# Kernel optimization log

Hardware: AMD Instinct MI355X
Metric: run time of the kernel (lower is better)

## Reference

```python
import jax, jax.numpy as jnp
import numpy as np
from math import factorial, pi, sqrt

N_ATOMS = 4096
N_PAIRS = 49152
F = 16           # num_tensordense_features
NUM_RADIAL = 16  # basis num=16
NUM_SPECIES = 95
EMB_DIM = 32
CUTOFF = 5.0
LMAX = 4         # SelfAttention max_degree=4
NLM = 25
LMAX_B = 2       # basis max_degree=2 (also max_tensordense_degree)
NLM_B = 9

DEG9 = np.repeat(np.arange(3), [1, 3, 5])        # degree index of each lm, l<=2
DEG25 = np.repeat(np.arange(5), [1, 3, 5, 7, 9]) # degree index of each lm, l<=4


def real_sph(u, lmax):
    # real spherical harmonics (m = -l..l ordering, no Condon-Shortley), u: (...,3) unit vectors
    x, y, z = u[..., 0], u[..., 1], u[..., 2]
    phi = jnp.arctan2(y, x)
    ct = jnp.clip(z, -1.0, 1.0)
    st = jnp.sqrt(jnp.clip(1.0 - ct * ct, 0.0, 1.0))
    P = {(0, 0): jnp.ones_like(ct)}
    for m in range(1, lmax + 1):
        P[(m, m)] = -(2 * m - 1) * st * P[(m - 1, m - 1)]
    for m in range(0, lmax):
        P[(m + 1, m)] = (2 * m + 1) * ct * P[(m, m)]
    for m in range(0, lmax + 1):
        for l in range(m + 2, lmax + 1):
            P[(l, m)] = ((2 * l - 1) * ct * P[(l - 1, m)] - (l + m - 1) * P[(l - 2, m)]) / (l - m)
    outs = []
    for l in range(lmax + 1):
        for m in range(-l, l + 1):
            ma = abs(m)
            Nn = sqrt((2 * l + 1) / (4 * pi) * factorial(l - ma) / factorial(l + ma))
            cs = (-1.0) ** ma  # cancel Condon-Shortley in P
            if m == 0:
                Y = Nn * P[(l, 0)]
            elif m > 0:
                Y = sqrt(2.0) * Nn * cs * jnp.cos(m * phi) * P[(l, m)]
            else:
                Y = sqrt(2.0) * Nn * cs * jnp.sin(ma * phi) * P[(l, ma)]
            outs.append(Y)
    return jnp.stack(outs, axis=-1)


def _gaunt():
    # exact real Gaunt (CG-equivalent) coupling coefficients via Gauss-Legendre x uniform-phi quadrature
    nt, nph = 16, 32
    xs, ws = np.polynomial.legendre.leggauss(nt)
    phis = np.arange(nph) * (2 * np.pi / nph)
    ct = np.repeat(xs, nph); ph = np.tile(phis, nt)
    st = np.sqrt(np.clip(1.0 - ct ** 2, 0.0, 1.0))
    u = np.stack([st * np.cos(ph), st * np.sin(ph), ct], -1)
    w = np.repeat(ws, nph) * (2 * np.pi / nph)
    Y = np.asarray(real_sph(jnp.asarray(u, dtype=jnp.float32), LMAX))
    G = np.einsum('gi,gj,gk,g->ijk', Y, Y[:, :NLM_B], Y, w)
    G[np.abs(G) < 1e-6] = 0.0
    return G

_G = _gaunt()
G_ATT = jnp.asarray(_G, dtype=jnp.float32)                      # (25, 9, 25): feat x basis -> feat
G_TD = jnp.asarray(_G[:NLM_B, :, :NLM_B], dtype=jnp.float32)    # (9, 9, 9): TensorDense coupling


def pdense(x, W, deg):
    return jnp.einsum('plf,lfg->plg', x, W[deg])


def couple(xf, Bf, G):
    # equivariant tensor product  out[p,k,f] = sum_ij G[i,j,k] xf[p,i,f] Bf[p,j,f]
    u = jnp.einsum('pif,ijk->pjkf', xf, G)
    return jnp.einsum('pjf,pjkf->pkf', Bf, u)


def setup_inputs() -> dict:
    key = jax.random.key(0)
    ks = jax.random.split(key, 24)
    s = 1.0 / np.sqrt(F)
    inp = dict(
        atomic_numbers=jax.random.randint(ks[0], (N_ATOMS,), 0, NUM_SPECIES),
        neighbour_indices=jnp.stack([
            jax.random.randint(ks[1], (N_PAIRS,), 0, N_ATOMS),
            jax.random.randint(ks[2], (N_PAIRS,), 0, N_ATOMS)], axis=-1),
        neighbour_displacements=jax.random.normal(ks[3], (N_PAIRS, 3), dtype=jnp.float32) * 1.7,
        W_rad=jax.random.normal(ks[4], (NUM_SPECIES, NUM_RADIAL, F), dtype=jnp.float32) / np.sqrt(NUM_RADIAL),
        emb_table=jax.random.normal(ks[5], (NUM_SPECIES, EMB_DIM), dtype=jnp.float32),
        W_emb=jax.random.normal(ks[6], (EMB_DIM, F), dtype=jnp.float32) / np.sqrt(EMB_DIM),
        b_emb=jnp.zeros((F,), jnp.float32),
        td_W1=jax.random.normal(ks[7], (3, F, F), dtype=jnp.float32) * s,
        td_W2=jax.random.normal(ks[8], (3, F, F), dtype=jnp.float32) * s,
        td_W3=jax.random.normal(ks[9], (3, F, F), dtype=jnp.float32) * s,
        Wb1=jax.random.normal(ks[10], (NUM_RADIAL, F), dtype=jnp.float32) / np.sqrt(NUM_RADIAL),
        Wq1=jax.random.normal(ks[11], (5, F, F), dtype=jnp.float32) * s,
        Wk1=jax.random.normal(ks[12], (5, F, F), dtype=jnp.float32) * s,
        Wv1=jax.random.normal(ks[13], (5, F, F), dtype=jnp.float32) * s,
        Wo1=jax.random.normal(ks[14], (5, F, F), dtype=jnp.float32) * s,
        bo1=jnp.zeros((F,), jnp.float32),
        Wb2=jax.random.normal(ks[15], (NUM_RADIAL, F), dtype=jnp.float32) / np.sqrt(NUM_RADIAL),
        Wq2=jax.random.normal(ks[16], (5, F, F), dtype=jnp.float32) * s,
        Wk2=jax.random.normal(ks[17], (5, F, F), dtype=jnp.float32) * s,
        Wv2=jax.random.normal(ks[18], (5, F, F), dtype=jnp.float32) * s,
        Wo2=jax.random.normal(ks[19], (5, F, F), dtype=jnp.float32) * s,
        bo2=jnp.zeros((F,), jnp.float32),
    )
    return inp


def reference(atomic_numbers, neighbour_indices, neighbour_displacements,
              W_rad, emb_table, W_emb, b_emb, td_W1, td_W2, td_W3,
              Wb1, Wq1, Wk1, Wv1, Wo1, bo1, Wb2, Wq2, Wk2, Wv2, Wo2, bo2):
    dst = neighbour_indices[:, 0]   # idx_i
    src = neighbour_indices[:, 1]   # idx_j
    Zj = atomic_numbers[src]
    r = jnp.linalg.norm(neighbour_displacements, axis=-1)
    u = neighbour_displacements / jnp.maximum(r, 1e-9)[:, None]
    sh = real_sph(u, LMAX)          # (P, 25)
    sh_b = sh[:, :NLM_B]            # (P, 9)
    kk = jnp.arange(1, NUM_RADIAL + 1, dtype=jnp.float32)
    rb = jnp.sinc(kk[None, :] * r[:, None] / CUTOFF) * (r < CUTOFF)[:, None]  # sinc basis w/ cutoff
    # species-aware radial basis -> per-pair equivariant features (P, 9, F)
    y0 = jnp.einsum('pk,pkf->pf', rb, W_rad[Zj])
    y = sh_b[:, :, None] * y0[:, None, :]
    # TensorDense: dense -> CG tensor product -> dense (degrees <= 2)
    a = pdense(y, td_W1, DEG9)
    b = pdense(y, td_W2, DEG9)
    u9 = jnp.einsum('pif,ijk->pjkf', a, G_TD)
    tp = jnp.einsum('pjf,pjkf->pkf', b, u9)
    y = pdense(tp, td_W3, DEG9)
    # aggregate per-pair messages to atoms (segment mean), pad degrees to l<=4
    sums = jnp.zeros((N_ATOMS, NLM_B, F), y.dtype).at[dst].add(y)
    cnt = jnp.zeros((N_ATOMS,), y.dtype).at[dst].add(1.0)
    x = sums / jnp.maximum(cnt, 1.0)[:, None, None]
    x = jnp.pad(x, ((0, 0), (0, NLM - NLM_B), (0, 0)))  # (N, 25, F)
    # two segment self-attention layers over neighbour pairs
    for (Wb, Wq, Wk, Wv, Wo, bo) in ((Wb1, Wq1, Wk1, Wv1, Wo1, bo1), (Wb2, Wq2, Wk2, Wv2, Wo2, bo2)):
        Bf = sh_b[:, :, None] * (rb @ Wb)[:, None, :]   # projected pair basis (P, 9, F)
        q = pdense(x, Wq, DEG25)[dst]
        kf = couple(pdense(x, Wk, DEG25)[src], Bf, G_ATT)
        vf = couple(pdense(x, Wv, DEG25)[src], Bf, G_ATT)
        s = jnp.einsum('plf,plf->p', q, kf) / np.sqrt(NLM * F)
        m = jax.lax.stop_gradient(jnp.full((N_ATOMS,), -1e30, s.dtype).at[dst].max(s))
        e = jnp.exp(s - m[dst])
        den = jnp.zeros((N_ATOMS,), s.dtype).at[dst].add(e)
        alpha = e / (den[dst] + 1e-9)
        agg = jnp.zeros((N_ATOMS, NLM, F), x.dtype).at[dst].add(alpha[:, None, None] * vf)
        x = pdense(agg, Wo, DEG25)
        x = x.at[:, 0, :].add(bo)
    # embedding residual connection on the scalar (l=0) channel
    res = emb_table[atomic_numbers] @ W_emb + b_emb
    x = x.at[:, 0, :].add(res)
    return x
```

## Files before the change

### kernel.cpp

```cpp
#include <hip/hip_runtime.h>
#include <hip/hip_bf16.h>

#define NA 4096
#define NP 49152

typedef _Float16 f16;
typedef _Float16 h2 __attribute__((ext_vector_type(2)));
union U4H { uint4 u; f16 h[8]; h2 p[4]; };

__device__ __forceinline__ float fdot2(h2 a, h2 b, float c){
#if __has_builtin(__builtin_amdgcn_fdot2)
  return __builtin_amdgcn_fdot2(a, b, c, false);
#else
  return c + (float)a.x*(float)b.x + (float)a.y*(float)b.y;
#endif
}

constexpr int WS_AOFS9 = 64;
constexpr int WS_ATTW9 = 128;
constexpr int WS_ATTIJ9= WS_ATTW9 + 512;
constexpr int WS_G     = 12800;
constexpr int WS_NATT  = WS_G + 5632;
constexpr int WS_ATTW  = WS_NATT + 8;
constexpr int WS_ATTIJ = WS_ATTW + 1024;
constexpr int WS_TDOFS = WS_ATTIJ + 1024;
constexpr int WS_TDW   = WS_TDOFS + 16;
constexpr int WS_TDIJ  = WS_TDW + 512;
constexpr int WS_AOFS  = WS_TDIJ + 512;
constexpr int WS_SH    = WS_AOFS + 32;
constexpr int WS_RB    = WS_SH + NP*9;
constexpr int WS_S     = WS_RB + NP*16;
constexpr int WS_CCNT  = WS_S + NP;
constexpr int WS_COFF  = WS_CCNT + NA;
constexpr int WS_CCUR  = WS_COFF + NA + 8;
constexpr int WS_CLST  = WS_CCUR + NA;
constexpr int WS_XQ    = WS_CLST + NP;
constexpr int WS_XK    = WS_XQ + NA*400;
constexpr int WS_XV    = WS_XK + NA*400;
constexpr int WS_PVF   = WS_XV + NA*400;
constexpr int WS_WW    = WS_PVF + NP*128;
constexpr int WS_PVFE  = WS_PVF + NP*256;
constexpr int WS_DS    = WS_PVFE;
constexpr long long WS_END = (long long)WS_DS + 2*NP + 16;

__device__ const float  GLX[16] = {
  -0.98940093499164993f, -0.94457502307323258f, -0.86563120238783174f, -0.75540440835500303f,
  -0.61787624440264375f, -0.45801677765722739f, -0.28160355077925891f, -0.09501250983763744f,
   0.09501250983763744f,  0.28160355077925891f,  0.45801677765722739f,  0.61787624440264375f,
   0.75540440835500303f,  0.86563120238783174f,  0.94457502307323258f,  0.98940093499164993f };
__device__ const double GLW[16] = {
  0.02715245941175409, 0.06225352393864789, 0.09515851168249278, 0.12462897125553387,
  0.14959598881657673, 0.16915651939500254, 0.18260341504492359, 0.18945061045506850,
  0.18945061045506850, 0.18260341504492359, 0.16915651939500254, 0.14959598881657673,
  0.12462897125553387, 0.09515851168249278, 0.06225352393864789, 0.02715245941175409 };

#define PI_D 3.14159265358979323846

__device__ __forceinline__ float scrub(float v){
  if(!(v == v)) return 0.f;
  return fminf(fmaxf(v, -1e30f), 1e30f);
}

__device__ void real_sph25(float ct, float phi, float* Y){
  float st = sqrtf(fmaxf(0.f, 1.f - ct*ct));
  float P[5][5];
  P[0][0] = 1.f;
  #pragma unroll
  for(int m=1;m<=4;m++) P[m][m] = -(2.f*m - 1.f)*st*P[m-1][m-1];
  #pragma unroll
  for(int m=0;m<4;m++) P[m+1][m] = (2.f*m + 1.f)*ct*P[m][m];
  #pragma unroll
  for(int m=0;m<=4;m++){
    #pragma unroll
    for(int l=m+2;l<=4;l++)
      P[l][m] = ((2.f*l - 1.f)*ct*P[l-1][m] - (float)(l+m-1)*P[l-2][m]) / (float)(l-m);
  }
  const double fact[9] = {1,1,2,6,24,120,720,5040,40320};
  int idx = 0;
  #pragma unroll
  for(int l=0;l<=4;l++){
    #pragma unroll
    for(int m=-l;m<=l;m++){
      int ma = (m < 0) ? -m : m;
      float Nn = (float)sqrt((2*l+1)/(4.0*PI_D)*fact[l-ma]/fact[l+ma]);
      float cs = (ma & 1) ? -1.f : 1.f;
      float v;
      if(m == 0)      v = Nn * P[l][0];
      else if(m > 0)  v = 1.4142135623730951f * Nn * cs * cosf(ma*phi) * P[l][ma];
      else            v = 1.4142135623730951f * Nn * cs * sinf(ma*phi) * P[l][ma];
      Y[idx++] = v;
    }
  }
}

__global__ __launch_bounds__(256) void k_u1(const float* Wrad, const float* W1,
    const float* W2, const int* nbr, float* ws){
  __shared__ float Ysh[12800];
  int b = blockIdx.x, tid = threadIdx.x;
  if(b < 176){
    for(int pt=tid; pt<512; pt+=256){
      float ct  = GLX[pt >> 5];
      float phi = (float)((pt & 31) * (2.0*PI_D/32.0));
      float Y[25];
      real_sph25(ct, phi, Y);
      #pragma unroll
      for(int i=0;i<25;i++) Ysh[pt*25 + i] = Y[i];
    }
    __syncthreads();
    int idx = b*256 + tid;
    int t = idx >> 3, chunk = idx & 7;
    if(t >= 5625) return;
    int k = t % 25, j = (t/25) % 9, i = t/225;
    double acc = 0.0;
    int g0 = chunk*64;
    #pragma unroll 4
    for(int g=g0; g<g0+64; g++){
      double w = GLW[g >> 5] * (2.0*PI_D/32.0);
      acc += w * (double)Ysh[g*25+i] * (double)Ysh[g*25+j] * (double)Ysh[g*25+k];
    }
    acc += __shfl_xor(acc, 1, 8);
    acc += __shfl_xor(acc, 2, 8);
    acc += __shfl_xor(acc, 4, 8);
    if(chunk == 0){
      if(fabs(acc) < 1e-6) acc = 0.0;
      ws[WS_G + (i*9+j)*25 + k] = (float)acc;
    }
  } else if(b < 271){
    int s = b - 176;
    #pragma unroll
    for(int it=0; it<6; it++){
      int idx = tid + 256*it;
      int w = idx / 768, r = idx % 768;
      int d = r / 256, r2 = r % 256, k = r2 / 16, g = r2 % 16;
      const float* Wsrc = (w == 0) ? W1 : W2;
      float acc = 0.f;
      #pragma unroll
      for(int fp=0; fp<16; fp++)
        acc += Wrad[(s*16+k)*16+fp] * Wsrc[(d*16+fp)*16+g];
      ws[WS_WW + ((size_t)(s*2+w)*16 + g)*48 + d*16 + k] = acc;
    }
  } else {
    int p = (b-271)*256 + tid;
    if(p < NP) atomicAdd((int*)ws + WS_CCNT + nbr[2*p], 1);
  }
}

__global__ __launch_bounds__(1024) void k_scan(float* ws){
  __shared__ int part[1024];
  int t = threadIdx.x;
  const int* cnt = (const int*)ws + WS_CCNT;
  int v0 = cnt[4*t], v1 = cnt[4*t+1], v2 = cnt[4*t+2], v3 = cnt[4*t+3];
  part[t] = v0+v1+v2+v3;
  __syncthreads();
  for(int o=1; o<1024; o<<=1){
    int x = (t >= o) ? part[t-o] : 0;
    __syncthreads();
    part[t] += x;
    __syncthreads();
  }
  int base = (t > 0) ? part[t-1] : 0;
  int* offp = (int*)ws + WS_COFF;
  int* cur  = (int*)ws + WS_CCUR;
  offp[4*t]   = base;          cur[4*t]   = base;
  offp[4*t+1] = base+v0;       cur[4*t+1] = base+v0;
  offp[4*t+2] = base+v0+v1;    cur[4*t+2] = base+v0+v1;
  offp[4*t+3] = base+v0+v1+v2; cur[4*t+3] = base+v0+v1+v2;
  if(t == 1023) offp[4096] = part[1023];
}

__global__ __launch_bounds__(256) void k_u2(const float* disp, const int* nbr, float* ws){
  __shared__ float Gsh[5632];
  __shared__ int cA[25], cT[9], cA9[25], oA[26], oT[10], oA9[26];
  if(blockIdx.x == 0){
    int t = threadIdx.x;
    for(int i=t; i<5625; i+=256) Gsh[i] = ws[WS_G + i];
    __syncthreads();
    const float* G = Gsh;
    if(t < 25){
      int c=0, c9=0;
      for(int i=0;i<25;i++) for(int j=0;j<9;j++) if(G[(i*9+j)*25+t] != 0.f){ c++; if(i<9) c9++; }
      cA[t]=c; cA9[t]=c9;
    }
    if(t < 9){ int c=0; for(int i=0;i<9;i++) for(int j=0;j<9;j++) if(G[(i*9+j)*25+t] != 0.f) c++; cT[t]=c; }
    __syncthreads();
    if(t == 0){
      int s=0; for(int k=0;k<25;k++){ oA[k]=s; s+=cA[k]; } oA[25]=s;
      ((int*)ws)[WS_NATT] = s;
      s=0; for(int k=0;k<25;k++){ oA9[k]=s; s+=cA9[k]; } oA9[25]=s;
      s=0; for(int k=0;k<9;k++){ oT[k]=s; s+=cT[k]; } oT[9]=s;
    }
    __syncthreads();
    float* attw = ws + WS_ATTW;  int* attij = (int*)ws + WS_ATTIJ;
    float* attw9 = ws + WS_ATTW9; int* attij9 = (int*)ws + WS_ATTIJ9;
    int* aofs  = (int*)ws + WS_AOFS;
    int* aofs9 = (int*)ws + WS_AOFS9;
    if(t < 26){ aofs[t] = oA[t] < 1024 ? oA[t] : 1024; aofs9[t] = oA9[t] < 512 ? oA9[t] : 512; }
    if(t < 25){
      int pos = oA[t], pos9 = oA9[t];
      for(int i=0;i<25;i++) for(int j=0;j<9;j++){
        float w = G[(i*9+j)*25+t];
        if(w != 0.f){
          if(pos < 1024){ attw[pos]=w; attij[pos] = i | (j<<5) | (t<<9); pos++; }
          if(i < 9 && pos9 < 512){ attw9[pos9]=w; attij9[pos9] = i | (j<<5) | (t<<9); pos9++; }
        }
      }
    }
    float* tdw = ws + WS_TDW; int* tdij = (int*)ws + WS_TDIJ; int* tdofs = (int*)ws + WS_TDOFS;
    if(t < 9){
      int pos = oT[t];
      for(int i=0;i<9;i++) for(int j=0;j<9;j++){
        float w = G[(i*9+j)*25+t];
        if(w != 0.f && pos < 512){
          int li = (i==0)?0:(i<4)?1:2, lj = (j==0)?0:(j<4)?1:2;
          tdw[pos]=w; tdij[pos] = i | (j<<5) | (li<<10) | (lj<<12); pos++;
        }
      }
      tdofs[t] = oT[t];
      if(t == 0) tdofs[9] = oT[9];
    }
  } else {
    int p = (blockIdx.x-1)*256 + threadIdx.x;
    if(p >= NP) return;
    int d = nbr[2*p], s = nbr[2*p+1];
    int sp = atomicAdd((int*)ws + WS_CCUR + d, 1);
    ((int*)ws)[WS_DS + 2*sp]     = d;
    ((int*)ws)[WS_DS + 2*sp + 1] = s;
    float dx = disp[3*p], dy = disp[3*p+1], dz = disp[3*p+2];
    float r = sqrtf(dx*dx + dy*dy + dz*dz);
    float inv = 1.f / fmaxf(r, 1e-9f);
    float ux = dx*inv, uy = dy*inv, uz = dz*inv;
    float sh[9];
    sh[0] = 0.28209479177387814f;
    sh[1] = 0.4886025119029199f * uy;
    sh[2] = 0.4886025119029199f * uz;
    sh[3] = 0.4886025119029199f * ux;
    sh[4] = 1.0925484305920792f * ux*uy;
    sh[5] = 1.0925484305920792f * uy*uz;
    sh[6] = 0.31539156525252005f * (3.f*uz*uz - 1.f);
    sh[7] = 1.0925484305920792f * ux*uz;
    sh[8] = 0.5462742152960396f * (ux*ux - uy*uy);
    #pragma unroll
    for(int i=0;i<9;i++) ws[WS_SH + sp*9 + i] = scrub(sh[i]);
    float mask = (r < 5.f) ? 1.f : 0.f;
    float rbv[16];
    #pragma unroll
    for(int k=1;k<=16;k++){
      float x  = (float)k * r * 0.2f;
      float px = 3.14159265358979323846f * x;
      float s2 = (px < 1e-6f) ? 1.f : (sinf(px)/px);
      rbv[k-1] = scrub(s2 * mask);
    }
    float4* rb4 = (float4*)(ws + WS_RB + sp*16);
    #pragma unroll
    for(int c=0;c<4;c++) rb4[c] = make_float4(rbv[4*c], rbv[4*c+1], rbv[4*c+2], rbv[4*c+3]);
  }
}

__global__ __launch_bounds__(256) void k_td(const int* aZ, const float* W3, float* ws){
  __shared__ float sh_s[16][9];
  __shared__ float S_s[16][88];
  __shared__ float tp_s[16][9][16];
  int tid = threadIdx.x, pl = tid >> 4, g = tid & 15;
  int sp = blockIdx.x*16 + pl;
  int src = ((const int*)ws)[WS_DS + 2*sp + 1];
  int Zj = aZ[src];
  {
    float4* S4 = (float4*)&S_s[0][0];
    for(int t0=tid; t0<352; t0+=256) S4[t0] = make_float4(0.f,0.f,0.f,0.f);
  }
  if(g < 9) sh_s[pl][g] = ws[WS_SH + sp*9 + g];
  float rb[16];
  {
    const float4* rb4 = (const float4*)(ws + WS_RB + sp*16);
    #pragma unroll
    for(int c=0;c<4;c++){
      float4 r = rb4[c];
      rb[4*c]=r.x; rb[4*c+1]=r.y; rb[4*c+2]=r.z; rb[4*c+3]=r.w;
    }
  }
  float A1[3], A2[3];
  {
    const float4* w1 = (const float4*)(ws + WS_WW + ((size_t)(Zj*2+0)*16+g)*48);
    const float4* w2 = (const float4*)(ws + WS_WW + ((size_t)(Zj*2+1)*16+g)*48);
    #pragma unroll
    for(int d=0; d<3; d++){
      float a1 = 0.f, a2 = 0.f;
      #pragma unroll
      for(int c=0;c<4;c++){
        float4 x1 = w1[d*4+c], x2 = w2[d*4+c];
        a1 += x1.x*rb[4*c] + x1.y*rb[4*c+1] + x1.z*rb[4*c+2] + x1.w*rb[4*c+3];
        a2 += x2.x*rb[4*c] + x2.y*rb[4*c+1] + x2.z*rb[4*c+2] + x2.w*rb[4*c+3];
      }
      A1[d] = a1; A2[d] = a2;
    }
  }
  __syncthreads();
  if(g < 9){
    const float* tdw = ws + WS_TDW;
    const int* tdij  = (const int*)ws + WS_TDIJ;
    const int* tdofs = (const int*)ws + WS_TDOFS;
    int e1 = tdofs[g+1];
    for(int e=tdofs[g]; e<e1; e++){
      float w = tdw[e]; int meta = tdij[e];
      int i = meta & 31, j = (meta>>5) & 15, li = (meta>>10) & 3, lj = (meta>>12) & 3;
      S_s[pl][g*9 + li*3 + lj] += w * sh_s[pl][i] * sh_s[pl][j];
    }
  }
  __syncthreads();
  float AA[9];
  #pragma unroll
  for(int li=0;li<3;li++)
    #pragma unroll
    for(int lj=0;lj<3;lj++) AA[li*3+lj] = A1[li]*A2[lj];
  #pragma unroll
  for(int k=0;k<9;k++){
    float tpv = 0.f;
    #pragma unroll
    for(int c=0;c<9;c++) tpv += S_s[pl][k*9+c] * AA[c];
    tp_s[pl][k][g] = tpv;
  }
  __syncthreads();
  float w3r[48];
  #pragma unroll
  for(int d=0;d<3;d++)
    #pragma unroll
    for(int f2=0;f2<16;f2++) w3r[d*16+f2] = W3[(d*16+f2)*16+g];
  float acc9[9];
  #pragma unroll
  for(int k=0;k<9;k++){
    int d = (k==0)?0:(k<4)?1:2;
    const float4* t4 = (const float4*)&tp_s[pl][k][0];
    float acc = 0.f;
    #pragma unroll
    for(int c=0;c<4;c++){
      float4 t = t4[c];
      acc += t.x*w3r[d*16+4*c] + t.y*w3r[d*16+4*c+1] + t.z*w3r[d*16+4*c+2] + t.w*w3r[d*16+4*c+3];
    }
    acc9[k] = scrub(acc);
  }
  f16* ptd = (f16*)(ws + WS_PVF) + (size_t)sp*256 + g*16;
  U4H u0, u1;
  #pragma unroll
  for(int j=0;j<8;j++) u0.h[j] = (f16)acc9[j];
  u1.h[0] = (f16)acc9[8];
  #pragma unroll
  for(int j=1;j<8;j++) u1.h[j] = (f16)0.f;
  *(uint4*)(ptd)     = u0.u;
  *(uint4*)(ptd + 8) = u1.u;
}

__global__ __launch_bounds__(256) void k_tdq(const float* Wq, const float* Wk,
                                             const float* Wv, float* ws){
  __shared__ float xsh[4][144];
  __shared__ float wq_sh[768], wk_sh[768], wv_sh[768];
  int tid = threadIdx.x, al = tid >> 6, lane = tid & 63;
  int a = blockIdx.x*4 + al;
  for(int t=tid; t<768; t+=256){ wq_sh[t]=Wq[t]; wk_sh[t]=Wk[t]; wv_sh[t]=Wv[t]; }
  const int* coff = (const int*)ws + WS_COFF;
  int off0 = coff[a], n = coff[a+1] - off0;
  const f16* base = (const f16*)(ws + WS_PVF);
  float acc[8] = {0,0,0,0,0,0,0,0};
  if(lane < 32){
    for(int t=0; t<n; t++){
      U4H u; u.u = *(const uint4*)(base + (size_t)(off0+t)*256 + lane*8);
      #pragma unroll
      for(int j=0;j<8;j++) acc[j] += (float)u.h[j];
    }
  }
  float invn = 1.f / fmaxf((float)n, 1.f);
  if(lane < 32){
    int gg = lane >> 1;
    #pragma unroll
    for(int j=0;j<8;j++){
      int k = (lane & 1)*8 + j;
      if(k < 9) xsh[al][k*16 + gg] = scrub(acc[j]*invn);
    }
  }
  __syncthreads();
  int g = lane & 15, q4 = lane >> 4;
  f16* qt = (f16*)(ws + WS_XQ) + (size_t)a*800 + g*32;
  f16* kt = (f16*)(ws + WS_XK) + (size_t)a*800 + g*32;
  f16* vt = (f16*)(ws + WS_XV) + (size_t)a*800 + g*32;
  for(int i=q4; i<9; i+=4){
    int l = (i==0)?0:(i<4)?1:2;
    float q=0.f, k2=0.f, v2=0.f;
    #pragma unroll
    for(int f2=0;f2<16;f2++){
      float xv = xsh[al][i*16+f2];
      q  += xv*wq_sh[(l*16+f2)*16+g];
      k2 += xv*wk_sh[(l*16+f2)*16+g];
      v2 += xv*wv_sh[(l*16+f2)*16+g];
    }
    qt[i] = (f16)q; kt[i] = (f16)k2; vt[i] = (f16)v2;
  }
}

template<int NI>
__global__ __launch_bounds__(128) void k_att(const float* Wb, float* ws){
  constexpr int MROWH = (NI == 9) ? 16 : 32;
  constexpr int PLSTR = (NI == 9) ? 408 : 840;
  __shared__ __align__(16) f16 Ml[8][PLSTR];
  __shared__ float sh_s[8][9];
  __shared__ float wb_sh[256];
  constexpr int NPAIR = NI/2;
  constexpr int TAIL  = NI-1;
  int tid = threadIdx.x, pl = tid >> 4, g = tid & 15;
  int sp = blockIdx.x*8 + pl;
  {
    uint4 z; z.x=0; z.y=0; z.z=0; z.w=0;
    uint4* Mz = (uint4*)&Ml[0][0];
    for(int t0=tid; t0<PLSTR; t0+=128) Mz[t0] = z;
  }
  for(int t0=tid; t0<256; t0+=128) wb_sh[t0] = Wb[t0];
  if(g < 9) sh_s[pl][g] = ws[WS_SH + sp*9 + g];
  __syncthreads();
  {
    const float* attw = ws + (NI==9 ? WS_ATTW9 : WS_ATTW);
    const int* attij  = (const int*)ws + (NI==9 ? WS_ATTIJ9 : WS_ATTIJ);
    const int* aofs   = (const int*)ws + (NI==9 ? WS_AOFS9 : WS_AOFS);
    for(int kr=g; kr<25; kr+=16){
      f16* Mrow = &Ml[pl][kr*MROWH];
      int e = aofs[kr], e1 = aofs[kr+1];
      if(e < e1){
        int meta = attij[e];
        int curi = meta & 31;
        float cur = 0.f;
        for(; e<e1; e++){
          meta = attij[e];
          int i2 = meta & 31;
          if(i2 != curi){ Mrow[curi] = (f16)cur; cur = 0.f; curi = i2; }
          cur += attw[e] * sh_s[pl][(meta>>5) & 15];
        }
        Mrow[curi] = (f16)cur;
      }
    }
  }
  __syncthreads();
  int dst = ((const int*)ws)[WS_DS + 2*sp];
  int src = ((const int*)ws)[WS_DS + 2*sp + 1];
  float q_r[NI];
  {
    const f16* qt = (const f16*)(ws + WS_XQ) + (size_t)dst*800 + g*32;
    #pragma unroll
    for(int c=0;c<NPAIR/4;c++){
      U4H u; u.u = *(const uint4*)(qt + c*8);
      #pragma unroll
      for(int j=0;j<8;j++) q_r[c*8+j] = (float)u.h[j];
    }
    q_r[TAIL] = (float)qt[TAIL];
  }
  h2 xk2[NPAIR], xv2[NPAIR];
  float xkT, xvT;
  {
    const f16* kt = (const f16*)(ws + WS_XK) + (size_t)src*800 + g*32;
    const f16* vt = (const f16*)(ws + WS_XV) + (size_t)src*800 + g*32;
    #pragma unroll
    for(int c=0;c<NPAIR/4;c++){
      U4H uk; uk.u = *(const uint4*)(kt + c*8);
      U4H uv; uv.u = *(const uint4*)(vt + c*8);
      #pragma unroll
      for(int j=0;j<4;j++){ xk2[c*4+j] = uk.p[j]; xv2[c*4+j] = uv.p[j]; }
    }
    xkT = (float)kt[TAIL];
    xvT = (float)vt[TAIL];
  }
  float wbf;
  {
    const float4* rb4 = (const float4*)(ws + WS_RB + sp*16);
    float acc = 0.f;
    #pragma unroll
    for(int c=0;c<4;c++){
      float4 r = rb4[c];
      acc += r.x*wb_sh[(4*c)*16+g] + r.y*wb_sh[(4*c+1)*16+g]
           + r.z*wb_sh[(4*c+2)*16+g] + r.w*wb_sh[(4*c+3)*16+g];
    }
    wbf = acc;
  }
  f16* pvf = (f16*)(ws + WS_PVF) + (size_t)sp*400;
  float sacc = 0.f;
  #pragma unroll
  for(int k=0;k<25;k++){
    const uint4* Mq = (const uint4*)&Ml[pl][k*MROWH];
    float mT = (float)Ml[pl][k*MROWH + TAIL];
    float vv0 = 0.f, vv1 = 0.f, kf0 = 0.f, kf1 = 0.f;
    #pragma unroll
    for(int c=0;c<NPAIR/4;c++){
      U4H u; u.u = Mq[c];
      vv0 = fdot2(u.p[0], xv2[c*4+0], vv0);
      vv1 = fdot2(u.p[1], xv2[c*4+1], vv1);
      vv0 = fdot2(u.p[2], xv2[c*4+2], vv0);
      vv1 = fdot2(u.p[3], xv2[c*4+3], vv1);
      if(k < NI){
        kf0 = fdot2(u.p[0], xk2[c*4+0], kf0);
        kf1 = fdot2(u.p[1], xk2[c*4+1], kf1);
        kf0 = fdot2(u.p[2], xk2[c*4+2], kf0);
        kf1 = fdot2(u.p[3], xk2[c*4+3], kf1);
      }
    }
    float vv = vv0 + vv1 + mT*xvT;
    if(k < NI){
      float kf = kf0 + kf1 + mT*xkT;
      sacc += q_r[k]*kf;
    }
    pvf[k*16 + g] = (f16)scrub(wbf*vv);
  }
  float sl = sacc;
  #pragma unroll
  for(int off=1; off<16; off<<=1) sl += __shfl_xor(sl, off, 16);
  if(g == 0) ws[WS_S + sp] = scrub(sl * 0.05f);
}

template<bool FINAL>
__global__ __launch_bounds__(256) void k_aggo(const float* Wo, const float* bo,
    const int* aZ, const float* emb, const float* Wemb, const float* bemb,
    const float* Wq, const float* Wk, const float* Wv, float* ws, float* out){
  __shared__ float xsh[4][400];
  __shared__ float wo_sh[1280];
  __shared__ float wq_sh[FINAL?4:1280], wk_sh[FINAL?4:1280], wv_sh[FINAL?4:1280];
  __shared__ float osh[FINAL?4:1600];
  int tid = threadIdx.x, al = tid >> 6, lane = tid & 63;
  int a = blockIdx.x*4 + al;
  for(int t=tid; t<1280; t+=256){
    wo_sh[t] = Wo[t];
    if(!FINAL){ wq_sh[t]=Wq[t]; wk_sh[t]=Wk[t]; wv_sh[t]=Wv[t]; }
  }
  const int* coff = (const int*)ws + WS_COFF;
  int off0 = coff[a], n = coff[a+1] - off0;
  float mx = -1e30f;
  for(int t=lane; t<n; t+=64) mx = fmaxf(mx, ws[WS_S + off0 + t]);
  #pragma unroll
  for(int off=1; off<64; off<<=1) mx = fmaxf(mx, __shfl_xor(mx, off));
  float den = 0.f;
  for(int t=lane; t<n; t+=64) den += expf(fminf(ws[WS_S + off0 + t] - mx, 0.f));
  #pragma unroll
  for(int off=1; off<64; off<<=1) den += __shfl_xor(den, off);
  float inv_den = 1.f / (den + 1e-9f);
  float acc[8] = {0,0,0,0,0,0,0,0};
  const f16* base = (const f16*)(ws + WS_PVF);
  for(int t=0; t<n; t++){
    float alpha = expf(fminf(ws[WS_S + off0 + t] - mx, 0.f)) * inv_den;
    if(lane < 50){
      U4H u; u.u = *(const uint4*)(base + (size_t)(off0+t)*400 + lane*8);
      #pragma unroll
      for(int j=0;j<8;j++) acc[j] += alpha * (float)u.h[j];
    }
  }
  if(lane < 50){
    #pragma unroll
    for(int j=0;j<8;j++) xsh[al][lane*8 + j] = scrub(acc[j]);
  }
  __syncthreads();
  int g = lane & 15, q4 = lane >> 4;
  for(int i=q4; i<25; i+=4){
    int l = (i==0)?0:(i<4)?1:(i<9)?2:(i<16)?3:4;
    float accv = 0.f;
    #pragma unroll
    for(int f2=0;f2<16;f2++) accv += xsh[al][i*16+f2]*wo_sh[(l*16+f2)*16+g];
    if(i == 0){
      accv += bo[g];
      if(FINAL){
        int Z = aZ[a];
        float res = bemb[g];
        #pragma unroll
        for(int e2=0;e2<32;e2++) res += emb[Z*32+e2]*Wemb[e2*16+g];
        accv += res;
      }
    }
    if(FINAL) out[a*400 + i*16 + g] = scrub(accv);
    else      osh[al*400 + i*16 + g] = scrub(accv);
  }
  if(!FINAL){
    __syncthreads();
    f16* qt = (f16*)(ws + WS_XQ) + (size_t)a*800 + g*32;
    f16* kt = (f16*)(ws + WS_XK) + (size_t)a*800 + g*32;
    f16* vt = (f16*)(ws + WS_XV) + (size_t)a*800 + g*32;
    for(int i=q4; i<25; i+=4){
      int l = (i==0)?0:(i<4)?1:(i<9)?2:(i<16)?3:4;
      float q=0.f, k2=0.f, v2=0.f;
      #pragma unroll
      for(int f2=0;f2<16;f2++){
        float xv = osh[al*400 + i*16 + f2];
        q  += xv*wq_sh[(l*16+f2)*16+g];
        k2 += xv*wk_sh[(l*16+f2)*16+g];
        v2 += xv*wv_sh[(l*16+f2)*16+g];
      }
      qt[i] = (f16)q; kt[i] = (f16)k2; vt[i] = (f16)v2;
    }
  }
}

extern "C" void kernel_launch(void* const* d_in, const int* in_sizes, int n_in,
                              void* d_out, int out_size, void* d_ws, size_t ws_size,
                              hipStream_t stream){
  (void)in_sizes; (void)n_in; (void)out_size;
  if(ws_size < (size_t)WS_END * sizeof(float)) return;
  float* ws = (float*)d_ws;
  const int* aZ  = (const int*)d_in[0];
  const int* nbr = (const int*)d_in[1];
  const float* disp = (const float*)d_in[2];
  const float* Wrad = (const float*)d_in[3];
  const float* emb  = (const float*)d_in[4];
  const float* Wemb = (const float*)d_in[5];
  const float* bemb = (const float*)d_in[6];
  const float* W1   = (const float*)d_in[7];
  const float* W2   = (const float*)d_in[8];
  const float* W3   = (const float*)d_in[9];
  const float* Wb1 = (const float*)d_in[10]; const float* Wq1 = (const float*)d_in[11];
  const float* Wk1 = (const float*)d_in[12]; const float* Wv1 = (const float*)d_in[13];
  const float* Wo1 = (const float*)d_in[14]; const float* bo1 = (const float*)d_in[15];
  const float* Wb2 = (const float*)d_in[16]; const float* Wq2 = (const float*)d_in[17];
  const float* Wk2 = (const float*)d_in[18]; const float* Wv2 = (const float*)d_in[19];
  const float* Wo2 = (const float*)d_in[20]; const float* bo2 = (const float*)d_in[21];

  hipMemsetAsync(ws + WS_CCNT, 0, NA*sizeof(int), stream);
  k_u1<<<463,256,0,stream>>>(Wrad, W1, W2, nbr, ws);
  k_scan<<<1,1024,0,stream>>>(ws);
  k_u2<<<193,256,0,stream>>>(disp, nbr, ws);
  k_td<<<3072,256,0,stream>>>(aZ, W3, ws);
  k_tdq<<<1024,256,0,stream>>>(Wq1, Wk1, Wv1, ws);

  k_att<9><<<6144,128,0,stream>>>(Wb1, ws);
  k_aggo<false><<<1024,256,0,stream>>>(Wo1, bo1, aZ, emb, Wemb, bemb,
                                       Wq2, Wk2, Wv2, ws, nullptr);
  k_att<25><<<6144,128,0,stream>>>(Wb2, ws);
  k_aggo<true><<<1024,256,0,stream>>>(Wo2, bo2, aZ, emb, Wemb, bemb,
                                      nullptr, nullptr, nullptr, ws, (float*)d_out);
}
```

Before: 390.3 us.

## Split attention pair work across 32 lanes, halving output rows per thread

Each pair in k_att is now handled by 32 threads instead of 16. Each half-group computes 13 of the 25 output rows, with the score reduced across 32 lanes, and the grid is doubled to 12288 blocks of 4 pairs each. The coupling-matrix build now gives one row per lane instead of looping. k_tdq zero-pads the layer-1 q/k/v entries 9..15 so the 9-degree kernel can load two full uint4 chunks and drop the tail handling. The aim is more parallelism and shorter per-thread serial chains, at the cost of redundant k/v loads per half and a wider shuffle reduction.

```diff
diff --git a/kernel.cpp b/kernel.cpp
--- a/kernel.cpp
+++ b/kernel.cpp
@@ -381,17 +381,21 @@
   f16* qt = (f16*)(ws + WS_XQ) + (size_t)a*800 + g*32;
   f16* kt = (f16*)(ws + WS_XK) + (size_t)a*800 + g*32;
   f16* vt = (f16*)(ws + WS_XV) + (size_t)a*800 + g*32;
-  for(int i=q4; i<9; i+=4){
-    int l = (i==0)?0:(i<4)?1:2;
-    float q=0.f, k2=0.f, v2=0.f;
-    #pragma unroll
-    for(int f2=0;f2<16;f2++){
-      float xv = xsh[al][i*16+f2];
-      q  += xv*wq_sh[(l*16+f2)*16+g];
-      k2 += xv*wk_sh[(l*16+f2)*16+g];
-      v2 += xv*wv_sh[(l*16+f2)*16+g];
-    }
-    qt[i] = (f16)q; kt[i] = (f16)k2; vt[i] = (f16)v2;
+  for(int i=q4; i<16; i+=4){
+    if(i < 9){
+      int l = (i==0)?0:(i<4)?1:2;
+      float q=0.f, k2=0.f, v2=0.f;
+      #pragma unroll
+      for(int f2=0;f2<16;f2++){
+        float xv = xsh[al][i*16+f2];
+        q  += xv*wq_sh[(l*16+f2)*16+g];
+        k2 += xv*wk_sh[(l*16+f2)*16+g];
+        v2 += xv*wv_sh[(l*16+f2)*16+g];
+      }
+      qt[i] = (f16)q; kt[i] = (f16)k2; vt[i] = (f16)v2;
+    } else {
+      qt[i] = (f16)0.f; kt[i] = (f16)0.f; vt[i] = (f16)0.f;
+    }
   }
 }
 
@@ -399,70 +403,63 @@
 __global__ __launch_bounds__(128) void k_att(const float* Wb, float* ws){
   constexpr int MROWH = (NI == 9) ? 16 : 32;
   constexpr int PLSTR = (NI == 9) ? 408 : 840;
-  __shared__ __align__(16) f16 Ml[8][PLSTR];
-  __shared__ float sh_s[8][9];
+  constexpr int NU4   = (NI == 9) ? 2 : 3;
+  __shared__ __align__(16) f16 Ml[4][PLSTR];
+  __shared__ float sh_s[4][9];
   __shared__ float wb_sh[256];
-  constexpr int NPAIR = NI/2;
-  constexpr int TAIL  = NI-1;
-  int tid = threadIdx.x, pl = tid >> 4, g = tid & 15;
-  int sp = blockIdx.x*8 + pl;
+  int tid = threadIdx.x, pl = tid >> 5, l32 = tid & 31, g = l32 & 15, half = l32 >> 4;
+  int sp = blockIdx.x*4 + pl;
   {
     uint4 z; z.x=0; z.y=0; z.z=0; z.w=0;
     uint4* Mz = (uint4*)&Ml[0][0];
-    for(int t0=tid; t0<PLSTR; t0+=128) Mz[t0] = z;
+    for(int t0=tid; t0<PLSTR/2; t0+=128) Mz[t0] = z;
   }
   for(int t0=tid; t0<256; t0+=128) wb_sh[t0] = Wb[t0];
-  if(g < 9) sh_s[pl][g] = ws[WS_SH + sp*9 + g];
-  __syncthreads();
-  {
+  if(l32 < 9) sh_s[pl][l32] = ws[WS_SH + sp*9 + l32];
+  __syncthreads();
+  if(l32 < 25){
     const float* attw = ws + (NI==9 ? WS_ATTW9 : WS_ATTW);
     const int* attij  = (const int*)ws + (NI==9 ? WS_ATTIJ9 : WS_ATTIJ);
     const int* aofs   = (const int*)ws + (NI==9 ? WS_AOFS9 : WS_AOFS);
-    for(int kr=g; kr<25; kr+=16){
-      f16* Mrow = &Ml[pl][kr*MROWH];
-      int e = aofs[kr], e1 = aofs[kr+1];
-      if(e < e1){
-        int meta = attij[e];
-        int curi = meta & 31;
-        float cur = 0.f;
-        for(; e<e1; e++){
-          meta = attij[e];
-          int i2 = meta & 31;
-          if(i2 != curi){ Mrow[curi] = (f16)cur; cur = 0.f; curi = i2; }
-          cur += attw[e] * sh_s[pl][(meta>>5) & 15];
-        }
-        Mrow[curi] = (f16)cur;
-      }
+    f16* Mrow = &Ml[pl][l32*MROWH];
+    int e = aofs[l32], e1 = aofs[l32+1];
+    if(e < e1){
+      int meta = attij[e];
+      int curi = meta & 31;
+      float cur = 0.f;
+      for(; e<e1; e++){
+        meta = attij[e];
+        int i2 = meta & 31;
+        if(i2 != curi){ Mrow[curi] = (f16)cur; cur = 0.f; curi = i2; }
+        cur += attw[e] * sh_s[pl][(meta>>5) & 15];
+      }
+      Mrow[curi] = (f16)cur;
     }
   }
   __syncthreads();
   int dst = ((const int*)ws)[WS_DS + 2*sp];
   int src = ((const int*)ws)[WS_DS + 2*sp + 1];
-  float q_r[NI];
+  int kbase = half*13;
+  float q_r[13];
   {
-    const f16* qt = (const f16*)(ws + WS_XQ) + (size_t)dst*800 + g*32;
-    #pragma unroll
-    for(int c=0;c<NPAIR/4;c++){
-      U4H u; u.u = *(const uint4*)(qt + c*8);
-      #pragma unroll
-      for(int j=0;j<8;j++) q_r[c*8+j] = (float)u.h[j];
-    }
-    q_r[TAIL] = (float)qt[TAIL];
-  }
-  h2 xk2[NPAIR], xv2[NPAIR];
+    const f16* qt = (const f16*)(ws + WS_XQ) + (size_t)dst*800 + g*32 + kbase;
+    #pragma unroll
+    for(int idx=0; idx<13; idx++) q_r[idx] = (float)qt[idx];
+  }
+  h2 xk2[NU4*4], xv2[NU4*4];
   float xkT, xvT;
   {
     const f16* kt = (const f16*)(ws + WS_XK) + (size_t)src*800 + g*32;
     const f16* vt = (const f16*)(ws + WS_XV) + (size_t)src*800 + g*32;
     #pragma unroll
-    for(int c=0;c<NPAIR/4;c++){
+    for(int c=0;c<NU4;c++){
       U4H uk; uk.u = *(const uint4*)(kt + c*8);
       U4H uv; uv.u = *(const uint4*)(vt + c*8);
       #pragma unroll
       for(int j=0;j<4;j++){ xk2[c*4+j] = uk.p[j]; xv2[c*4+j] = uv.p[j]; }
     }
-    xkT = (float)kt[TAIL];
-    xvT = (float)vt[TAIL];
+    if(NI == 25){ xkT = (float)kt[24]; xvT = (float)vt[24]; }
+    else        { xkT = 0.f; xvT = 0.f; }
   }
   float wbf;
   {
@@ -479,35 +476,33 @@
   f16* pvf = (f16*)(ws + WS_PVF) + (size_t)sp*400;
   float sacc = 0.f;
   #pragma unroll
-  for(int k=0;k<25;k++){
-    const uint4* Mq = (const uint4*)&Ml[pl][k*MROWH];
-    float mT = (float)Ml[pl][k*MROWH + TAIL];
-    float vv0 = 0.f, vv1 = 0.f, kf0 = 0.f, kf1 = 0.f;
-    #pragma unroll
-    for(int c=0;c<NPAIR/4;c++){
-      U4H u; u.u = Mq[c];
-      vv0 = fdot2(u.p[0], xv2[c*4+0], vv0);
-      vv1 = fdot2(u.p[1], xv2[c*4+1], vv1);
-      vv0 = fdot2(u.p[2], xv2[c*4+2], vv0);
-      vv1 = fdot2(u.p[3], xv2[c*4+3], vv1);
-      if(k < NI){
-        kf0 = fdot2(u.p[0], xk2[c*4+0], kf0);
-        kf1 = fdot2(u.p[1], xk2[c*4+1], kf1);
-        kf0 = fdot2(u.p[2], xk2[c*4+2], kf0);
-        kf1 = fdot2(u.p[3], xk2[c*4+3], kf1);
-      }
-    }
-    float vv = vv0 + vv1 + mT*xvT;
-    if(k < NI){
-      float kf = kf0 + kf1 + mT*xkT;
-      sacc += q_r[k]*kf;
-    }
-    pvf[k*16 + g] = (f16)scrub(wbf*vv);
+  for(int idx=0; idx<13; idx++){
+    if(!(half == 1 && idx == 12)){
+      int k = kbase + idx;
+      const uint4* Mq = (const uint4*)&Ml[pl][k*MROWH];
+      float vv = 0.f, kf = 0.f;
+      #pragma unroll
+      for(int c=0;c<NU4;c++){
+        U4H u; u.u = Mq[c];
+        #pragma unroll
+        for(int j=0;j<4;j++){
+          vv = fdot2(u.p[j], xv2[c*4+j], vv);
+          if(k < NI) kf = fdot2(u.p[j], xk2[c*4+j], kf);
+        }
+      }
+      if(NI == 25){
+        float mT = (float)Ml[pl][k*MROWH + 24];
+        vv += mT*xvT;
+        kf += mT*xkT;
+      }
+      if(k < NI) sacc += q_r[idx]*kf;
+      pvf[k*16 + g] = (f16)scrub(wbf*vv);
+    }
   }
   float sl = sacc;
   #pragma unroll
-  for(int off=1; off<16; off<<=1) sl += __shfl_xor(sl, off, 16);
-  if(g == 0) ws[WS_S + sp] = scrub(sl * 0.05f);
+  for(int off=1; off<32; off<<=1) sl += __shfl_xor(sl, off, 32);
+  if(l32 == 0) ws[WS_S + sp] = scrub(sl * 0.05f);
 }
 
 template<bool FINAL>
@@ -619,10 +614,10 @@
   k_td<<<3072,256,0,stream>>>(aZ, W3, ws);
   k_tdq<<<1024,256,0,stream>>>(Wq1, Wk1, Wv1, ws);
 
-  k_att<9><<<6144,128,0,stream>>>(Wb1, ws);
+  k_att<9><<<12288,128,0,stream>>>(Wb1, ws);
   k_aggo<false><<<1024,256,0,stream>>>(Wo1, bo1, aZ, emb, Wemb, bemb,
                                        Wq2, Wk2, Wv2, ws, nullptr);
-  k_att<25><<<6144,128,0,stream>>>(Wb2, ws);
+  k_att<25><<<12288,128,0,stream>>>(Wb2, ws);
   k_aggo<true><<<1024,256,0,stream>>>(Wo2, bo2, aZ, emb, Wemb, bemb,
                                       nullptr, nullptr, nullptr, ws, (float*)d_out);
 }
```

After: 424.1 us. +8.6%, slower.
